# Performance work log

Hardware: AMD Instinct MI355X
Metric: run time of the kernel (lower is better)

## Reference

```python
import jax, jax.numpy as jnp
import numpy as np
from jax import lax

B, CIN, COUT, K, S, P, H, W = 8, 128, 256, 3, 1, 1, 64, 64


def setup_inputs() -> dict:
    key = jax.random.key(0)
    k1, k2, k3, k4, k5 = jax.random.split(key, 5)
    fan_off = CIN * K * K
    fan_dc = CIN * K * K
    return {
        "x": jax.random.normal(k1, (B, CIN, H, W), dtype=jnp.float32),
        # offset-predicting conv: Conv2d(CIN, 2*K*K, K, S, P, padding_mode='reflect')
        "w_off": jax.random.normal(k2, (2 * K * K, CIN, K, K), dtype=jnp.float32) / np.sqrt(fan_off),
        "b_off": jax.random.normal(k3, (2 * K * K,), dtype=jnp.float32) * 0.01,
        # deformable conv weights: DeformConv2d(CIN, COUT, K, S, P)
        "w_dc": jax.random.normal(k4, (COUT, CIN, K, K), dtype=jnp.float32) / np.sqrt(fan_dc),
        "b_dc": jax.random.normal(k5, (COUT,), dtype=jnp.float32) * 0.01,
    }


def _reflect_conv(x, w, b, stride, pad):
    # Conv2d with reflect padding
    xp = jnp.pad(x, ((0, 0), (0, 0), (pad, pad), (pad, pad)), mode="reflect")
    y = lax.conv_general_dilated(xp, w, (stride, stride), "VALID",
                                 dimension_numbers=("NCHW", "OIHW", "NCHW"))
    return y + b[None, :, None, None]


def _deform_conv(x, offset, w, b, k, stride, pad):
    # torchvision DeformConv2d (v1, no mask, 1 offset group)
    Bn, C, Hi, Wi = x.shape
    Ho, Wo = offset.shape[2], offset.shape[3]
    KK = k * k
    # offset layout: [B, 2*KK, Ho, Wo], interleaved (dy, dx) per kernel position
    off = offset.reshape(Bn, KK, 2, Ho, Wo)
    hb = jnp.arange(Ho, dtype=x.dtype) * stride - pad          # base rows
    wb = jnp.arange(Wo, dtype=x.dtype) * stride - pad          # base cols
    ki, kj = jnp.meshgrid(jnp.arange(k, dtype=x.dtype), jnp.arange(k, dtype=x.dtype), indexing="ij")
    ki, kj = ki.reshape(KK), kj.reshape(KK)
    # sampling locations [B, KK, Ho, Wo]
    py = off[:, :, 0] + hb[None, None, :, None] + ki[None, :, None, None]
    px = off[:, :, 1] + wb[None, None, None, :] + kj[None, :, None, None]
    y0 = jnp.floor(py)
    x0 = jnp.floor(px)
    dy = (py - y0).reshape(Bn, 1, -1)
    dx = (px - x0).reshape(Bn, 1, -1)
    y0i = y0.astype(jnp.int32)
    x0i = x0.astype(jnp.int32)
    xf = x.reshape(Bn, C, Hi * Wi)

    def gather(yi, xi):
        valid = (yi >= 0) & (yi < Hi) & (xi >= 0) & (xi < Wi)
        yc = jnp.clip(yi, 0, Hi - 1)
        xc = jnp.clip(xi, 0, Wi - 1)
        idx = (yc * Wi + xc).reshape(Bn, -1)                   # [B, KK*Ho*Wo]
        g = jax.vmap(lambda xb, ib: xb[:, ib])(xf, idx)        # [B, C, KK*Ho*Wo]
        return g * valid.reshape(Bn, 1, -1).astype(x.dtype)

    v00 = gather(y0i, x0i)
    v01 = gather(y0i, x0i + 1)
    v10 = gather(y0i + 1, x0i)
    v11 = gather(y0i + 1, x0i + 1)
    vals = (v00 * (1 - dy) * (1 - dx) + v01 * (1 - dy) * dx
            + v10 * dy * (1 - dx) + v11 * dy * dx)             # [B, C, KK*Ho*Wo]
    cols = vals.reshape(Bn, C, KK, Ho * Wo)
    out = jnp.einsum("bckl,ock->bol", cols, w.reshape(-1, C, KK))
    out = out + b[None, :, None]
    return out.reshape(Bn, -1, Ho, Wo)


def reference(x, w_off, b_off, w_dc, b_dc):
    x_offset = _reflect_conv(x, w_off, b_off, S, P)            # [B, 2*K*K, Ho, Wo]
    # torch.chunk followed by torch.concat is an identity on the offset tensor
    return _deform_conv(x, x_offset, w_dc, b_dc, K, S, P)
```

## Files before the change

### kernel.cpp

```cpp
#include <hip/hip_runtime.h>
#include <hip/hip_fp16.h>

typedef unsigned short u16;
typedef unsigned int   u32;
typedef u32   u32x2  __attribute__((ext_vector_type(2)));
typedef u32   u32x4  __attribute__((ext_vector_type(4)));
typedef short short8 __attribute__((ext_vector_type(8)));
typedef float f32x4  __attribute__((ext_vector_type(4)));
typedef _Float16 half8 __attribute__((ext_vector_type(8)));

__device__ __forceinline__ u16 f2h(float f) { return __half_as_ushort(__float2half(f)); }
__device__ __forceinline__ f32x4 mfma16(short8 a, short8 b, f32x4 c) {
  return __builtin_amdgcn_mfma_f32_16x16x32_f16(
      __builtin_bit_cast(half8, a), __builtin_bit_cast(half8, b), c, 0, 0, 0);
}
__device__ __forceinline__ __half2 h2cast(u32 u) { return __builtin_bit_cast(__half2, u); }
__device__ __forceinline__ int refl(int v) { return v < 0 ? -v : (v > 63 ? 126 - v : v); }

__global__ __launch_bounds__(256) void prep_fused(const float* __restrict__ x,
                                                  const float* __restrict__ w_dc,
                                                  const float* __restrict__ w_off,
                                                  u16* __restrict__ xh,
                                                  u16* __restrict__ Wl2,
                                                  u16* __restrict__ Wol2) {
  int bid = blockIdx.x;
  int tid = threadIdx.x;
  if (bid < 512) {
    __shared__ float tile[128][65];
    int swz = (bid & 7) * 64 + (bid >> 3);
    int b = swz >> 6, h = swz & 63;
    for (int i = 0; i < 32; ++i) {
      int c = (tid >> 6) + i * 4;
      int w = tid & 63;
      tile[c][w] = x[(((size_t)b * 128 + c) * 64 + h) * 64 + w];
    }
    __syncthreads();
    u16* dst = xh + ((size_t)(b * 64 + h) * 64) * 128;
    for (int j = 0; j < 32; ++j) {
      int c = tid & 127;
      int w = (tid >> 7) + 2 * j;
      dst[w * 128 + c] = f2h(tile[c][w]);
    }
  } else {
    int idx = (bid - 512) * 256 + tid;
    if (idx < 294912) {
      int e = idx & 7, lane = (idx >> 3) & 63, ks = (idx >> 9) & 3;
      int mt = (idx >> 11) & 15, kk = idx >> 15;
      int o = mt * 16 + (lane & 15), c = ks * 32 + (lane >> 4) * 8 + e;
      Wl2[idx] = f2h(w_dc[(o * 128 + c) * 9 + kk]);
    } else {
      int i2 = idx - 294912;
      int e = i2 & 7, lane = (i2 >> 3) & 63, ks = (i2 >> 9) & 3;
      int mt = (i2 >> 11) & 1, kk = i2 >> 12;
      int co = mt * 16 + (lane & 15), c = ks * 32 + (lane >> 4) * 8 + e;
      Wol2[i2] = (co < 18) ? f2h(w_off[(co * 128 + c) * 9 + kk]) : (u16)0;
    }
  }
}

__device__ __forceinline__ void make_entry_lds(u32x4* __restrict__ tbl, int kk,
                                               int ho, int wo, float offy, float offx) {
  int ki = kk / 3, kj = kk - ki * 3;
  float py = offy + (float)(ho + ki - 1);
  float px = offx + (float)(wo + kj - 1);
  float fy0 = floorf(py), fx0 = floorf(px);
  int y0 = (int)fy0, x0 = (int)fx0;
  float fy = py - fy0, fx = px - fx0;
  float w11 = fy * fx, w10 = fy - w11, w01 = fx - w11, w00 = 1.f - fy - fx + w11;
  bool iy0 = (y0 >= 0) & (y0 < 64), iy1 = (y0 >= -1) & (y0 < 63);
  bool ix0 = (x0 >= 0) & (x0 < 64), ix1 = (x0 >= -1) & (x0 < 63);
  int y0c = min(max(y0, 0), 63), x0c = min(max(x0, 0), 63);
  u32 addr00 = (u32)((y0c * 64 + x0c) * 128);
  u32 dx = (x0 >= 0 && x0 < 63) ? 128u : 0u;
  u32 dy = (y0 >= 0 && y0 < 63) ? 8192u : 0u;
  u32 wA = (u32)f2h((iy0 && ix0) ? w00 : 0.f) | ((u32)f2h((iy0 && ix1) ? w01 : 0.f) << 16);
  u32 wB = (u32)f2h((iy1 && ix0) ? w10 : 0.f) | ((u32)f2h((iy1 && ix1) ? w11 : 0.f) << 16);
  u32x4 ent; ent.x = addr00; ent.y = dx | (dy << 16); ent.z = wA; ent.w = wB;
  tbl[kk * 64 + wo] = ent;
}

__global__ __launch_bounds__(512, 4) void deform_fused(
    const u16* __restrict__ xh, const u16* __restrict__ Wl2,
    const u16* __restrict__ Wol2, const float* __restrict__ b_off,
    const float* __restrict__ b_dc, float* __restrict__ out) {
  union SMU {
    u16 slab[3][64][128];
    struct { u16 cols[2][64][128]; u32x4 tbl[576]; } pb;
  };
  __shared__ SMU sm;
  int bid = blockIdx.x;
  int b = bid & 7, ho = bid >> 3;
  int tid = threadIdx.x, lane = tid & 63, wv = tid >> 6;
  int ln15 = lane & 15, kg = lane >> 4;
  const u16* xb = xh + (size_t)b * 524288;

  {
    u32x4 st[6];
#pragma unroll
    for (int i = 0; i < 6; ++i) {
      int T = tid + i * 512;
      int r = T >> 10, w = (T >> 4) & 63, cb = (T & 15) * 8;
      int hr = refl(ho + r - 1);
      st[i] = *(const u32x4*)(xb + (hr * 64 + w) * 128 + cb);
    }
#pragma unroll
    for (int i = 0; i < 6; ++i) {
      int T = tid + i * 512;
      int r = T >> 10, w = (T >> 4) & 63, cb = (T & 15) * 8;
      *(u32x4*)&sm.slab[r][w][cb ^ ((w & 7) << 3)] = st[i];
    }
  }
  __syncthreads();

  int mtA = wv & 1, ntA = wv >> 1;
  int lq = ntA * 16 + ln15;
  f32x4 oacc = {0.f, 0.f, 0.f, 0.f};
  __builtin_amdgcn_s_setprio(1);
#pragma unroll
  for (int kk = 0; kk < 9; ++kk) {
    int ki = kk / 3, kj = kk - ki * 3;
    int j = refl(lq + kj - 1);
    const u16* wb = Wol2 + ((kk * 2 + mtA) * 4) * 512 + lane * 8;
    int sbj = (j & 7) << 3;
#pragma unroll
    for (int ks = 0; ks < 4; ++ks) {
      short8 af = *(const short8*)(wb + ks * 512);
      short8 bf = *(const short8*)&sm.slab[ki][j][(ks * 32 + kg * 8) ^ sbj];
      oacc = mfma16(af, bf, oacc);
    }
  }
  __builtin_amdgcn_s_setprio(0);
  __syncthreads();

  if (mtA == 0) {
    int kkA = 2 * kg, kkB = 2 * kg + 1;
    make_entry_lds(sm.pb.tbl, kkA, ho, lq, oacc[0] + b_off[2 * kkA], oacc[1] + b_off[2 * kkA + 1]);
    make_entry_lds(sm.pb.tbl, kkB, ho, lq, oacc[2] + b_off[2 * kkB], oacc[3] + b_off[2 * kkB + 1]);
  } else if (kg == 0) {
    make_entry_lds(sm.pb.tbl, 8, ho, lq, oacc[0] + b_off[16], oacc[1] + b_off[17]);
  }
  __syncthreads();

  int tl0 = tid >> 4;
  int tcl = (tid & 15) * 8;
  int swzc = tcl ^ ((tl0 & 7) << 3);

  u32x4 gv[2][4];
  u32 gwAv[2], gwBv[2];
  auto gissue = [&](int g) {
#pragma unroll
    for (int i = 0; i < 2; ++i) {
      int l = tl0 + i * 32;
      u32x4 e = sm.pb.tbl[g * 64 + l];
      gwAv[i] = e.z; gwBv[i] = e.w;
      const u16* p = xb + e.x + tcl;
      u32 dxv = e.y & 0xffffu, dyv = e.y >> 16;
      gv[i][0] = *(const u32x4*)p;
      gv[i][1] = *(const u32x4*)(p + dxv);
      gv[i][2] = *(const u32x4*)(p + dyv);
      gv[i][3] = *(const u32x4*)(p + dyv + dxv);
    }
  };
  auto gwrite = [&](int dbuf) {
#pragma unroll
    for (int i = 0; i < 2; ++i) {
      int l = tl0 + i * 32;
      __half2 wA = h2cast(gwAv[i]), wB = h2cast(gwBv[i]);
      __half2 w00 = __half2half2(wA.x), w01 = __half2half2(wA.y);
      __half2 w10 = __half2half2(wB.x), w11 = __half2half2(wB.y);
      u32x4 pv;
#pragma unroll
      for (int wd = 0; wd < 4; ++wd) {
        __half2 r = __hmul2(h2cast(gv[i][0][wd]), w00);
        r = __hfma2(h2cast(gv[i][1][wd]), w01, r);
        r = __hfma2(h2cast(gv[i][2][wd]), w10, r);
        r = __hfma2(h2cast(gv[i][3][wd]), w11, r);
        pv[wd] = __builtin_bit_cast(u32, r);
      }
      *(u32x4*)&sm.pb.cols[dbuf][l][swzc] = pv;
    }
  };

  f32x4 acc[2][4];
#pragma unroll
  for (int m = 0; m < 2; ++m)
#pragma unroll
    for (int n = 0; n < 4; ++n) acc[m][n] = (f32x4){0.f, 0.f, 0.f, 0.f};

  gissue(0); gwrite(0);
  gissue(1);
  __syncthreads();

  int swzb = (ln15 & 7) << 3;
  for (int kk = 0; kk < 9; ++kk) {
    int cur = kk & 1;
    const u16* wbase = Wl2 + (size_t)kk * 32768 + lane * 8;
    short8 a[2][4];
#pragma unroll
    for (int mt = 0; mt < 2; ++mt)
#pragma unroll
      for (int ks = 0; ks < 4; ++ks)
        a[mt][ks] = *(const short8*)(wbase + (size_t)(((wv * 2 + mt) * 4) + ks) * 512);
    if (kk < 8) gwrite(cur ^ 1);
    if (kk < 7) gissue(kk + 2);
    __builtin_amdgcn_s_setprio(1);
#pragma unroll
    for (int ks = 0; ks < 4; ++ks) {
#pragma unroll
      for (int nt = 0; nt < 4; ++nt) {
        short8 bf = *(const short8*)&sm.pb.cols[cur][nt * 16 + ln15][(ks * 32 + kg * 8) ^ swzb];
#pragma unroll
        for (int mt = 0; mt < 2; ++mt)
          acc[mt][nt] = mfma16(a[mt][ks], bf, acc[mt][nt]);
      }
    }
    __builtin_amdgcn_s_setprio(0);
    __syncthreads();
  }

#pragma unroll
  for (int mt = 0; mt < 2; ++mt) {
#pragma unroll
    for (int r = 0; r < 4; ++r) {
      int o = wv * 32 + mt * 16 + kg * 4 + r;
      float bias = b_dc[o];
      size_t base = ((size_t)(b * 256 + o)) * 4096 + ho * 64;
#pragma unroll
      for (int nt = 0; nt < 4; ++nt) {
        out[base + nt * 16 + ln15] = acc[mt][nt][r] + bias;
      }
    }
  }
}

extern "C" void kernel_launch(void* const* d_in, const int* in_sizes, int n_in,
                              void* d_out, int out_size, void* d_ws, size_t ws_size,
                              hipStream_t stream) {
  const float* x     = (const float*)d_in[0];
  const float* w_off = (const float*)d_in[1];
  const float* b_off = (const float*)d_in[2];
  const float* w_dc  = (const float*)d_in[3];
  const float* b_dc  = (const float*)d_in[4];
  float* out = (float*)d_out;
  char* ws = (char*)d_ws;
  u16* xh   = (u16*)ws;
  u16* Wl2  = (u16*)(ws + 8388608);
  u16* Wol2 = (u16*)(ws + 8388608 + 589824);
  prep_fused  <<<dim3(1808), dim3(256), 0, stream>>>(x, w_dc, w_off, xh, Wl2, Wol2);
  deform_fused<<<dim3(512),  dim3(512), 0, stream>>>(xh, Wl2, Wol2, b_off, b_dc, out);
}
```

Measured before the change: 47.04 us.

## Split waves into dedicated gather producers and MFMA consumers

The block's waves are now specialised. Waves 4-7 only gather and bilinearly interpolate the deformable samples into the double-buffered LDS column tile. Waves 0-3 only run the MFMA GEMM, each covering 64 output channels instead of 32, and prefetch the next k-slice of weight fragments from global memory while the current one is multiplied. The aim is to overlap gather latency with tensor-core work instead of interleaving both in every wave. The cost is fewer MFMA waves, a larger accumulator register footprint per compute wave, and more gather registers per producer wave, which could reduce occupancy or leave the compute waves as the bottleneck.

New measurement: 45.74 us. 2.8% less time.

```diff
diff --git a/kernel.cpp b/kernel.cpp
--- a/kernel.cpp
+++ b/kernel.cpp
@@ -141,93 +141,108 @@
   }
   __syncthreads();
 
-  int tl0 = tid >> 4;
-  int tcl = (tid & 15) * 8;
-  int swzc = tcl ^ ((tl0 & 7) << 3);
-
-  u32x4 gv[2][4];
-  u32 gwAv[2], gwBv[2];
-  auto gissue = [&](int g) {
-#pragma unroll
-    for (int i = 0; i < 2; ++i) {
-      int l = tl0 + i * 32;
-      u32x4 e = sm.pb.tbl[g * 64 + l];
-      gwAv[i] = e.z; gwBv[i] = e.w;
-      const u16* p = xb + e.x + tcl;
-      u32 dxv = e.y & 0xffffu, dyv = e.y >> 16;
-      gv[i][0] = *(const u32x4*)p;
-      gv[i][1] = *(const u32x4*)(p + dxv);
-      gv[i][2] = *(const u32x4*)(p + dyv);
-      gv[i][3] = *(const u32x4*)(p + dyv + dxv);
-    }
-  };
-  auto gwrite = [&](int dbuf) {
-#pragma unroll
-    for (int i = 0; i < 2; ++i) {
-      int l = tl0 + i * 32;
-      __half2 wA = h2cast(gwAv[i]), wB = h2cast(gwBv[i]);
-      __half2 w00 = __half2half2(wA.x), w01 = __half2half2(wA.y);
-      __half2 w10 = __half2half2(wB.x), w11 = __half2half2(wB.y);
-      u32x4 pv;
-#pragma unroll
-      for (int wd = 0; wd < 4; ++wd) {
-        __half2 r = __hmul2(h2cast(gv[i][0][wd]), w00);
-        r = __hfma2(h2cast(gv[i][1][wd]), w01, r);
-        r = __hfma2(h2cast(gv[i][2][wd]), w10, r);
-        r = __hfma2(h2cast(gv[i][3][wd]), w11, r);
-        pv[wd] = __builtin_bit_cast(u32, r);
-      }
-      *(u32x4*)&sm.pb.cols[dbuf][l][swzc] = pv;
-    }
-  };
-
-  f32x4 acc[2][4];
-#pragma unroll
-  for (int m = 0; m < 2; ++m)
-#pragma unroll
-    for (int n = 0; n < 4; ++n) acc[m][n] = (f32x4){0.f, 0.f, 0.f, 0.f};
-
-  gissue(0); gwrite(0);
-  gissue(1);
-  __syncthreads();
-
-  int swzb = (ln15 & 7) << 3;
-  for (int kk = 0; kk < 9; ++kk) {
-    int cur = kk & 1;
-    const u16* wbase = Wl2 + (size_t)kk * 32768 + lane * 8;
-    short8 a[2][4];
-#pragma unroll
-    for (int mt = 0; mt < 2; ++mt)
-#pragma unroll
-      for (int ks = 0; ks < 4; ++ks)
-        a[mt][ks] = *(const short8*)(wbase + (size_t)(((wv * 2 + mt) * 4) + ks) * 512);
-    if (kk < 8) gwrite(cur ^ 1);
-    if (kk < 7) gissue(kk + 2);
-    __builtin_amdgcn_s_setprio(1);
-#pragma unroll
-    for (int ks = 0; ks < 4; ++ks) {
-#pragma unroll
-      for (int nt = 0; nt < 4; ++nt) {
-        short8 bf = *(const short8*)&sm.pb.cols[cur][nt * 16 + ln15][(ks * 32 + kg * 8) ^ swzb];
-#pragma unroll
-        for (int mt = 0; mt < 2; ++mt)
-          acc[mt][nt] = mfma16(a[mt][ks], bf, acc[mt][nt]);
-      }
-    }
-    __builtin_amdgcn_s_setprio(0);
+  if (wv >= 4) {
+    int pt = tid & 255;
+    int tl = pt >> 4;
+    int tcl = (pt & 15) * 8;
+    int swzc = tcl ^ ((tl & 7) << 3);
+
+    u32x4 gv[4][4];
+    u32 gwA[4], gwB[4];
+    auto gissue = [&](int g) {
+#pragma unroll
+      for (int i = 0; i < 4; ++i) {
+        int l = tl + i * 16;
+        u32x4 e = sm.pb.tbl[g * 64 + l];
+        gwA[i] = e.z; gwB[i] = e.w;
+        const u16* p = xb + e.x + tcl;
+        u32 dxv = e.y & 0xffffu, dyv = e.y >> 16;
+        gv[i][0] = *(const u32x4*)p;
+        gv[i][1] = *(const u32x4*)(p + dxv);
+        gv[i][2] = *(const u32x4*)(p + dyv);
+        gv[i][3] = *(const u32x4*)(p + dyv + dxv);
+      }
+    };
+    auto gwrite = [&](int dbuf) {
+#pragma unroll
+      for (int i = 0; i < 4; ++i) {
+        int l = tl + i * 16;
+        __half2 wA = h2cast(gwA[i]), wB = h2cast(gwB[i]);
+        __half2 w00 = __half2half2(wA.x), w01 = __half2half2(wA.y);
+        __half2 w10 = __half2half2(wB.x), w11 = __half2half2(wB.y);
+        u32x4 pv;
+#pragma unroll
+        for (int wd = 0; wd < 4; ++wd) {
+          __half2 r = __hmul2(h2cast(gv[i][0][wd]), w00);
+          r = __hfma2(h2cast(gv[i][1][wd]), w01, r);
+          r = __hfma2(h2cast(gv[i][2][wd]), w10, r);
+          r = __hfma2(h2cast(gv[i][3][wd]), w11, r);
+          pv[wd] = __builtin_bit_cast(u32, r);
+        }
+        *(u32x4*)&sm.pb.cols[dbuf][l][swzc] = pv;
+      }
+    };
+
+    gissue(0); gwrite(0);
+    gissue(1);
     __syncthreads();
-  }
-
-#pragma unroll
-  for (int mt = 0; mt < 2; ++mt) {
-#pragma unroll
-    for (int r = 0; r < 4; ++r) {
-      int o = wv * 32 + mt * 16 + kg * 4 + r;
-      float bias = b_dc[o];
-      size_t base = ((size_t)(b * 256 + o)) * 4096 + ho * 64;
-#pragma unroll
-      for (int nt = 0; nt < 4; ++nt) {
-        out[base + nt * 16 + ln15] = acc[mt][nt][r] + bias;
+    for (int kk = 0; kk < 9; ++kk) {
+      int cur = kk & 1;
+      if (kk < 8) gwrite(cur ^ 1);
+      if (kk < 7) gissue(kk + 2);
+      __syncthreads();
+    }
+  } else {
+    f32x4 acc[4][4];
+#pragma unroll
+    for (int m = 0; m < 4; ++m)
+#pragma unroll
+      for (int n = 0; n < 4; ++n) acc[m][n] = (f32x4){0.f, 0.f, 0.f, 0.f};
+
+    int swzb = (ln15 & 7) << 3;
+    __syncthreads();
+    for (int kk = 0; kk < 9; ++kk) {
+      int cur = kk & 1;
+      const u16* wb = Wl2 + (size_t)kk * 32768 + lane * 8;
+      short8 ac[4], an[4];
+#pragma unroll
+      for (int m = 0; m < 4; ++m)
+        ac[m] = *(const short8*)(wb + (size_t)((wv * 4 + m) * 4) * 512);
+#pragma unroll
+      for (int ks = 0; ks < 4; ++ks) {
+        if (ks < 3) {
+#pragma unroll
+          for (int m = 0; m < 4; ++m)
+            an[m] = *(const short8*)(wb + (size_t)((wv * 4 + m) * 4 + ks + 1) * 512);
+        }
+        __builtin_amdgcn_s_setprio(1);
+#pragma unroll
+        for (int nt = 0; nt < 4; ++nt) {
+          short8 bf = *(const short8*)&sm.pb.cols[cur][nt * 16 + ln15][(ks * 32 + kg * 8) ^ swzb];
+#pragma unroll
+          for (int m = 0; m < 4; ++m)
+            acc[m][nt] = mfma16(ac[m], bf, acc[m][nt]);
+        }
+        __builtin_amdgcn_s_setprio(0);
+        if (ks < 3) {
+#pragma unroll
+          for (int m = 0; m < 4; ++m) ac[m] = an[m];
+        }
+      }
+      __syncthreads();
+    }
+
+#pragma unroll
+    for (int m = 0; m < 4; ++m) {
+#pragma unroll
+      for (int r = 0; r < 4; ++r) {
+        int o = wv * 64 + m * 16 + kg * 4 + r;
+        float bias = b_dc[o];
+        size_t base = ((size_t)(b * 256 + o)) * 4096 + ho * 64;
+#pragma unroll
+        for (int nt = 0; nt < 4; ++nt) {
+          out[base + nt * 16 + ln15] = acc[m][nt][r] + bias;
+        }
       }
     }
   }
```
